# Kernel optimization log

Hardware: AMD Instinct MI355X
Metric: run time of the kernel (lower is better)

## Reference

```python
import jax, jax.numpy as jnp
import numpy as np
import math

EPS = 1e-6

def _rmsnorm(x, w):
    var = jnp.mean(x * x, axis=-1, keepdims=True)
    return x * jax.lax.rsqrt(var + EPS) * w

def _rotary(x, cos, sin):
    d = x.shape[-1] // 2
    x1, x2 = x[..., :d], x[..., d:]
    return jnp.concatenate([x1 * cos - x2 * sin, x2 * cos + x1 * sin], axis=-1)

def _conv1x1(x, w):
    # x: (B, C, 1, S), w: (O, C) -> (B, O, 1, S)
    return jnp.einsum('bcls,oc->bols', x, w)

def setup_inputs() -> dict:
    key = jax.random.key(0)
    ks = jax.random.split(key, 12)
    B, H, KVH, D, S, T, HID = 8, 16, 2, 128, 16, 8192, 2048
    return {
        'x': jax.random.normal(ks[0], (B, HID, 1, S), jnp.float32),
        'cos': jax.random.uniform(ks[1], (1, 1, S, D // 2), jnp.float32),
        'sin': jax.random.uniform(ks[2], (1, 1, S, D // 2), jnp.float32),
        'kv_cache_k': jax.random.normal(ks[3], (B, KVH, T, D), jnp.float32),
        'kv_cache_v': jax.random.normal(ks[4], (B, KVH, T, D), jnp.float32),
        'position': 4096,
        'mask': jnp.zeros((1, 1, S, T), jnp.float32),
        'wq': jax.random.normal(ks[5], (H * D, HID), jnp.float32) * 0.02,
        'wk': jax.random.normal(ks[6], (KVH * D, HID), jnp.float32) * 0.02,
        'wv': jax.random.normal(ks[7], (KVH * D, HID), jnp.float32) * 0.02,
        'wo': jax.random.normal(ks[8], (HID, H * D), jnp.float32) * 0.02,
        'q_norm_w': jnp.ones((D,), jnp.float32),
        'k_norm_w': jnp.ones((D,), jnp.float32),
    }

def reference(x, cos, sin, kv_cache_k, kv_cache_v, position, mask,
              wq, wk, wv, wo, q_norm_w, k_norm_w):
    B, S = x.shape[0], x.shape[3]
    D = q_norm_w.shape[0]
    H = wq.shape[0] // D
    KVH = wk.shape[0] // D
    G = H // KVH  # GQA group size

    # projections (1x1 conv == channel matmul), then (B, h, S, D)
    q = _conv1x1(x, wq)[:, :, 0, :].reshape(B, H, D, S).transpose(0, 1, 3, 2)
    k = _conv1x1(x, wk)[:, :, 0, :].reshape(B, KVH, D, S).transpose(0, 1, 3, 2)
    v = _conv1x1(x, wv)[:, :, 0, :].reshape(B, KVH, D, S).transpose(0, 1, 3, 2)

    q = _rotary(_rmsnorm(q, q_norm_w), cos, sin)
    k = _rotary(_rmsnorm(k, k_norm_w), cos, sin)

    # scatter new k/v into cache at `position`
    new_k = jax.lax.dynamic_update_slice(kv_cache_k, k, (0, 0, position, 0))
    new_v = jax.lax.dynamic_update_slice(kv_cache_v, v, (0, 0, position, 0))

    # GQA: fold q heads into (kv_head, group) so K/V need no repeat_interleave
    scale = 1.0 / math.sqrt(D)
    qg = q.reshape(B, KVH, G, S, D)
    attn = jnp.einsum('bkgsd,bktd->bkgst', qg, new_k) * scale
    attn = attn + mask[:, :, None, :, :]  # (1,1,S,T) -> broadcast over groups
    probs = jax.nn.softmax(attn, axis=-1)
    out = jnp.einsum('bkgst,bktd->bkgsd', probs, new_v).reshape(B, H, S, D)

    # back to (B, H*D, 1, S) and output projection
    out = out.transpose(0, 1, 3, 2).reshape(B, H * D, 1, S)
    out = _conv1x1(out, wo)
    return out, new_k, new_v
```

## Files before the change

### kernel.cpp

```cpp
#include <hip/hip_runtime.h>
#include <cstdint>
#include <cstddef>


typedef __attribute__((ext_vector_type(8))) short bf16x8;
typedef __attribute__((ext_vector_type(4))) float f32x4;
typedef unsigned short u16;
typedef unsigned int u32;

#define MFMA16(a, b, c) __builtin_amdgcn_mfma_f32_16x16x32_bf16(a, b, c, 0, 0, 0)

static __device__ __forceinline__ u16 f2bf(float f) {
  u32 u = __float_as_uint(f);
  u += 0x7FFFu + ((u >> 16) & 1u);
  return (u16)(u >> 16);
}
static __device__ __forceinline__ float bf2f(u16 u) {
  return __uint_as_float(((u32)u) << 16);
}
static __device__ __forceinline__ u32 pk2(float a, float b) {
  return (u32)f2bf(a) | ((u32)f2bf(b) << 16);
}

__global__ __launch_bounds__(256) void transpose_x(const float* __restrict__ x,
                                                   u16* __restrict__ Xt) {
  int id = blockIdx.x * 256 + threadIdx.x;
  int b = id >> 13, c = (id >> 2) & 2047, s4 = id & 3;
  float4 v = *(const float4*)(x + ((size_t)(b * 2048 + c)) * 16 + s4 * 4);
  size_t base = (size_t)(b * 16 + s4 * 4) * 2048 + c;
  Xt[base]        = f2bf(v.x);
  Xt[base + 2048] = f2bf(v.y);
  Xt[base + 4096] = f2bf(v.z);
  Xt[base + 6144] = f2bf(v.w);
}

template <int MODE>
__global__ __launch_bounds__(512) void gemm16(const float* __restrict__ w0,
                                              const float* __restrict__ w1,
                                              const float* __restrict__ w2,
                                              const u16* __restrict__ Bt,
                                              float* __restrict__ outp) {
  __shared__ __align__(16) u16 sW[2][16 * 256];
  __shared__ __align__(16) float sRed[2048];
  const int t512 = threadIdx.x;
  const int half = t512 >> 8;
  const int tid = t512 & 255;
  const int lane = tid & 63, w = tid >> 6;
  const int q = lane >> 4, n = lane & 15;
  const int m0 = blockIdx.x * 16;
  const float* wbase;
  if (MODE == 0) {
    if (m0 < 2048)      wbase = w0 + (size_t)m0 * 2048;
    else if (m0 < 2304) wbase = w1 + (size_t)(m0 - 2048) * 2048;
    else                wbase = w2 + (size_t)(m0 - 2304) * 2048;
  } else {
    wbase = w0 + (size_t)m0 * 2048;
  }
  const int kbase = half * 1024;
  f32x4 acc0 = {0.f, 0.f, 0.f, 0.f}, acc1 = acc0;

  for (int c0 = kbase; c0 < kbase + 1024; c0 += 256) {
    {
      int m = tid >> 4, s16 = tid & 15;
      const float* src = wbase + (size_t)m * 2048 + c0 + s16 * 16;
      float4 a = *(const float4*)(src);
      float4 b = *(const float4*)(src + 4);
      float4 c = *(const float4*)(src + 8);
      float4 d = *(const float4*)(src + 12);
      uint4 u0 = {pk2(a.x, a.y), pk2(a.z, a.w), pk2(b.x, b.y), pk2(b.z, b.w)};
      uint4 u1 = {pk2(c.x, c.y), pk2(c.z, c.w), pk2(d.x, d.y), pk2(d.z, d.w)};
      int G0 = 2 * s16;
      *(uint4*)&sW[half][m * 256 + ((G0 + m) & 31) * 8]     = u0;
      *(uint4*)&sW[half][m * 256 + ((G0 + 1 + m) & 31) * 8] = u1;
    }
    __syncthreads();
    bf16x8 bfr[2][8];
#pragma unroll
    for (int e = 0; e < 2; ++e) {
      int j = 32 * w + 16 * e + n;
      const u16* bp = Bt + (size_t)j * 2048 + c0 + q * 8;
#pragma unroll
      for (int ks = 0; ks < 8; ++ks) bfr[e][ks] = *(const bf16x8*)(bp + ks * 32);
    }
#pragma unroll
    for (int ks = 0; ks < 8; ++ks) {
      bf16x8 af = *(const bf16x8*)&sW[half][n * 256 + (((4 * ks + q) + n) & 31) * 8];
      acc0 = MFMA16(af, bfr[0][ks], acc0);
      acc1 = MFMA16(af, bfr[1][ks], acc1);
    }
    __syncthreads();
  }
  if (half == 1) {
    *(f32x4*)&sRed[tid * 8]     = acc0;
    *(f32x4*)&sRed[tid * 8 + 4] = acc1;
  }
  __syncthreads();
  if (half == 0) {
    acc0 += *(const f32x4*)&sRed[tid * 8];
    acc1 += *(const f32x4*)&sRed[tid * 8 + 4];
#pragma unroll
    for (int e = 0; e < 2; ++e) {
      f32x4 a = e ? acc1 : acc0;
      int j = 32 * w + 16 * e + n;
      if (MODE == 0) {
        *(f32x4*)&outp[(size_t)j * 2560 + m0 + 4 * q] = a;
      } else {
#pragma unroll
        for (int reg = 0; reg < 4; ++reg) {
          int m = m0 + 4 * q + reg;
          outp[(size_t)(j >> 4) * 32768 + m * 16 + (j & 15)] = a[reg];
        }
      }
    }
  }
}

__global__ __launch_bounds__(256) void norm_rot(
    const float* __restrict__ qkv, const float* __restrict__ cosb,
    const float* __restrict__ sinb, const float* __restrict__ qw,
    const float* __restrict__ kw,
    u16* __restrict__ Qa, float* __restrict__ knew, float* __restrict__ vnew) {
  const int wid = blockIdx.x * 4 + (threadIdx.x >> 6);
  const int lane = threadIdx.x & 63;
  const float SCALE = 0.08838834764831845f;
  if (wid < 2048) {
    int b = wid >> 8, h = (wid >> 4) & 15, s = wid & 15;
    int j = b * 16 + s;
    const float* row = qkv + (size_t)j * 2560 + h * 128;
    float v1 = row[lane];
    float v2 = row[lane + 64];
    float ss = v1 * v1 + v2 * v2;
#pragma unroll
    for (int o = 32; o > 0; o >>= 1) ss += __shfl_xor(ss, o, 64);
    float rr = rsqrtf(ss * (1.0f / 128.0f) + 1e-6f);
    float n1 = v1 * rr * qw[lane];
    float n2 = v2 * rr * qw[lane + 64];
    float c = cosb[s * 64 + lane], sn = sinb[s * 64 + lane];
    u16* dst = Qa + (size_t)((b * 16 + h) * 16 + s) * 128;
    dst[lane]      = f2bf((n1 * c - n2 * sn) * SCALE);
    dst[lane + 64] = f2bf((n2 * c + n1 * sn) * SCALE);
  } else if (wid < 2304) {
    int idx = wid - 2048;
    int b = idx >> 5, kvh = (idx >> 4) & 1, s = idx & 15;
    int j = b * 16 + s;
    const float* row = qkv + (size_t)j * 2560 + 2048 + kvh * 128;
    float v1 = row[lane];
    float v2 = row[lane + 64];
    float ss = v1 * v1 + v2 * v2;
#pragma unroll
    for (int o = 32; o > 0; o >>= 1) ss += __shfl_xor(ss, o, 64);
    float rr = rsqrtf(ss * (1.0f / 128.0f) + 1e-6f);
    float n1 = v1 * rr * kw[lane];
    float n2 = v2 * rr * kw[lane + 64];
    float c = cosb[s * 64 + lane], sn = sinb[s * 64 + lane];
    float* dst = knew + (size_t)((b * 2 + kvh) * 16 + s) * 128;
    dst[lane]      = n1 * c - n2 * sn;
    dst[lane + 64] = n2 * c + n1 * sn;
  } else {
    int idx = wid - 2304;
    int b = idx >> 5, kvh = (idx >> 4) & 1, s = idx & 15;
    int j = b * 16 + s;
    const float* row = qkv + (size_t)j * 2560 + 2304 + kvh * 128;
    float* dst = vnew + (size_t)((b * 2 + kvh) * 16 + s) * 128;
    dst[lane]      = row[lane];
    dst[lane + 64] = row[lane + 64];
  }
}

__global__ __launch_bounds__(256, 2) void attn(
    const u16* __restrict__ Qa, const float* __restrict__ kcache,
    const float* __restrict__ vcache, const float* __restrict__ knew,
    const float* __restrict__ vnew, const int* __restrict__ posp,
    const float* __restrict__ mask, float* __restrict__ outk,
    float* __restrict__ outv, u16* __restrict__ Opart,
    float* __restrict__ Mpart, float* __restrict__ Lpart) {
  __shared__ __align__(16) u16 lds[32768];

  const int tid = threadIdx.x, lane = tid & 63, w = tid >> 6;
  const int q = lane >> 4, n = lane & 15;
  const int bid = blockIdx.x;
  const int bk = bid >> 5, chunk = bid & 31;
  const int b = bk >> 1, kvh = bk & 1;
  const int pos = *posp;

  const int stl = tid >> 4;
  const int g = tid & 15;

#define SRC_PTR(isV_, tg_)                                                   \
  ((isV_) ? (((tg_) >= pos && (tg_) < pos + 16)                              \
                 ? (vnew + (size_t)(bk * 16 + ((tg_) - pos)) * 128)          \
                 : (vcache + ((size_t)bk * 8192 + (tg_)) * 128))             \
          : (((tg_) >= pos && (tg_) < pos + 16)                              \
                 ? (knew + (size_t)(bk * 16 + ((tg_) - pos)) * 128)          \
                 : (kcache + ((size_t)bk * 8192 + (tg_)) * 128)))

  float4 pf[8][2];
#define ISSUE_STAGE(tile_)                                                   \
  {                                                                          \
    const int t0_ = chunk * 256 + (tile_) * 64;                              \
    _Pragma("unroll") for (int u = 0; u < 8; ++u) {                          \
      int isV_ = u >> 2;                                                     \
      int tl_ = (stl + 16 * u) & 63;                                         \
      int tg_ = t0_ + tl_;                                                   \
      const float* s_ = SRC_PTR(isV_, tg_) + g * 8;                          \
      pf[u][0] = *(const float4*)(s_);                                       \
      pf[u][1] = *(const float4*)(s_ + 4);                                   \
    }                                                                        \
  }

  float4 mv4[4];
#define LOAD_MASK(tile_)                                                     \
  {                                                                          \
    const int t0_ = chunk * 256 + (tile_) * 64;                              \
    _Pragma("unroll") for (int mt = 0; mt < 4; ++mt)                         \
        mv4[mt] =                                                            \
        *(const float4*)(mask + (size_t)n * 8192 + t0_ + 16 * mt + 4 * q);   \
  }

  ISSUE_STAGE(0);

  bf16x8 qf[2][4];
#pragma unroll
  for (int e = 0; e < 2; ++e) {
    int r = 32 * w + 16 * e + n;
    int h = kvh * 8 + (r >> 4), s = r & 15;
    const u16* qrow = Qa + (size_t)((b * 16 + h) * 16 + s) * 128;
#pragma unroll
    for (int ks = 0; ks < 4; ++ks)
      qf[e][ks] = *(const bf16x8*)(qrow + (4 * ks + q) * 8);
  }

  LOAD_MASK(0);

  bf16x8 idE = {0, 0, 0, 0, 0, 0, 0, 0}, idO = idE;
  {
    const short one = (short)0x3F80;
    int tq = n >> 3, te = n & 7;
#pragma unroll
    for (int e = 0; e < 8; ++e) {
      if (q == tq && e == te) idE[e] = one;
      if (q == tq + 2 && e == te) idO[e] = one;
    }
  }

  float m_old[2] = {-INFINITY, -INFINITY}, l_old[2] = {0.f, 0.f};
  f32x4 oacc[2][8];
#pragma unroll
  for (int e = 0; e < 2; ++e)
#pragma unroll
    for (int nt = 0; nt < 8; ++nt) oacc[e][nt] = (f32x4){0.f, 0.f, 0.f, 0.f};

  for (int tile = 0; tile < 4; ++tile) {
    const int t0 = chunk * 256 + tile * 64;
#pragma unroll
    for (int u = 0; u < 8; ++u) {
      int isV = u >> 2;
      int tl = (stl + 16 * u) & 63;
      int tg = t0 + tl;
      float* dst = (isV ? outv : outk) + ((size_t)bk * 8192 + tg) * 128 + g * 8;
      float4 a = pf[u][0], b2 = pf[u][1];
      *(float4*)dst = a;
      *(float4*)(dst + 4) = b2;
      uint4 uu = {pk2(a.x, a.y), pk2(a.z, a.w), pk2(b2.x, b2.y), pk2(b2.z, b2.w)};
      *(uint4*)&lds[isV * 8192 + tl * 128 + ((g + tl) & 15) * 8] = uu;
    }
    __syncthreads();

    if (tile < 3) { ISSUE_STAGE(tile + 1); }

    f32x4 sacc[4][2];
#pragma unroll
    for (int mt = 0; mt < 4; ++mt) {
      sacc[mt][0] = (f32x4){0.f, 0.f, 0.f, 0.f};
      sacc[mt][1] = sacc[mt][0];
    }
#pragma unroll
    for (int ks = 0; ks < 4; ++ks) {
#pragma unroll
      for (int mt = 0; mt < 4; ++mt) {
        int trow = 16 * mt + n;
        bf16x8 kf = *(const bf16x8*)&lds[trow * 128 + (((4 * ks + q) + trow) & 15) * 8];
        sacc[mt][0] = MFMA16(kf, qf[0][ks], sacc[mt][0]);
        sacc[mt][1] = MFMA16(kf, qf[1][ks], sacc[mt][1]);
      }
    }

#pragma unroll
    for (int mtv = 0; mtv < 4; ++mtv) {
      int trow = 16 * mtv + n;
      bf16x8 vfr = *(const bf16x8*)&lds[8192 + trow * 128 + (((4 * w + q) + trow) & 15) * 8];
      f32x4 z = {0.f, 0.f, 0.f, 0.f};
      f32x4 d0 = MFMA16(vfr, idE, z);
      f32x4 d1 = MFMA16(vfr, idO, z);
      int G = 2 * mtv + (q >> 1), off = 4 * (q & 1);
      int dp0 = 32 * w + n, dp1 = dp0 + 16;
      uint2 u0 = {pk2(d0[0], d0[1]), pk2(d0[2], d0[3])};
      uint2 u1 = {pk2(d1[0], d1[1]), pk2(d1[2], d1[3])};
      *(uint2*)&lds[24576 + dp0 * 64 + ((G + dp0) & 7) * 8 + off] = u0;
      *(uint2*)&lds[24576 + dp1 * 64 + ((G + dp1) & 7) * 8 + off] = u1;
    }

    float al[2];
#pragma unroll
    for (int e = 0; e < 2; ++e) {
      float sv[4][4];
      float mx = -INFINITY;
#pragma unroll
      for (int mt = 0; mt < 4; ++mt)
#pragma unroll
        for (int rg = 0; rg < 4; ++rg) {
          float v = sacc[mt][e][rg] + mv4[mt][rg];
          sv[mt][rg] = v;
          mx = fmaxf(mx, v);
        }
      mx = fmaxf(mx, __shfl_xor(mx, 16));
      mx = fmaxf(mx, __shfl_xor(mx, 32));
      float mn = fmaxf(m_old[e], mx);
      al[e] = __expf(m_old[e] - mn);
      float ts = 0.f;
      int r = 32 * w + 16 * e + n;
#pragma unroll
      for (int mt = 0; mt < 4; ++mt) {
        float p0 = __expf(sv[mt][0] - mn), p1 = __expf(sv[mt][1] - mn);
        float p2 = __expf(sv[mt][2] - mn), p3 = __expf(sv[mt][3] - mn);
        ts += (p0 + p1) + (p2 + p3);
        uint2 up = {pk2(p0, p1), pk2(p2, p3)};
        int G = 2 * mt + (q >> 1), off = 4 * (q & 1);
        *(uint2*)&lds[16384 + r * 64 + ((G + r) & 7) * 8 + off] = up;
      }
      ts += __shfl_xor(ts, 16);
      ts += __shfl_xor(ts, 32);
      l_old[e] = l_old[e] * al[e] + ts;
      m_old[e] = mn;
    }
    if (tile < 3) { LOAD_MASK(tile + 1); }
    __syncthreads();

#pragma unroll
    for (int e = 0; e < 2; ++e) {
      float an[4];
#pragma unroll
      for (int rg = 0; rg < 4; ++rg) an[rg] = __shfl(al[e], 4 * q + rg);
#pragma unroll
      for (int nt = 0; nt < 8; ++nt)
#pragma unroll
        for (int rg = 0; rg < 4; ++rg) oacc[e][nt][rg] *= an[rg];
    }
    bf16x8 Pf[2][2];
#pragma unroll
    for (int e = 0; e < 2; ++e) {
      int r = 32 * w + 16 * e + n;
#pragma unroll
      for (int ks = 0; ks < 2; ++ks)
        Pf[e][ks] = *(const bf16x8*)&lds[16384 + r * 64 + (((4 * ks + q) + r) & 7) * 8];
    }
#pragma unroll
    for (int nt = 0; nt < 8; ++nt) {
      int d = 16 * nt + n;
#pragma unroll
      for (int ks = 0; ks < 2; ++ks) {
        bf16x8 vf = *(const bf16x8*)&lds[24576 + d * 64 + (((4 * ks + q) + d) & 7) * 8];
        oacc[0][nt] = MFMA16(Pf[0][ks], vf, oacc[0][nt]);
        oacc[1][nt] = MFMA16(Pf[1][ks], vf, oacc[1][nt]);
      }
    }
  }

#pragma unroll
  for (int e = 0; e < 2; ++e)
#pragma unroll
    for (int nt = 0; nt < 8; ++nt) {
      int d = 16 * nt + n;
      int r0 = 32 * w + 16 * e + 4 * q;
      int G = r0 >> 3, off = 4 * (q & 1);
      uint2 u = {pk2(oacc[e][nt][0], oacc[e][nt][1]),
                 pk2(oacc[e][nt][2], oacc[e][nt][3])};
      *(uint2*)&lds[d * 128 + ((G + d) & 15) * 8 + off] = u;
    }
  if (q == 0) {
#pragma unroll
    for (int e = 0; e < 2; ++e) {
      int r = 32 * w + 16 * e + n;
      Mpart[(size_t)bid * 128 + r] = m_old[e];
      Lpart[(size_t)bid * 128 + r] = l_old[e];
    }
  }
  __syncthreads();
  for (int i = tid; i < 2048; i += 256) {
    int d2 = i >> 4, g2 = i & 15;
    uint4 v = *(const uint4*)&lds[d2 * 128 + ((g2 + d2) & 15) * 8];
    *(uint4*)(Opart + (size_t)bid * 16384 + d2 * 128 + g2 * 8) = v;
  }
#undef SRC_PTR
#undef ISSUE_STAGE
#undef LOAD_MASK
}

__global__ __launch_bounds__(256) void combine(const u16* __restrict__ Opart,
                                               const float* __restrict__ Mp,
                                               const float* __restrict__ Lp,
                                               u16* __restrict__ A2t) {
  __shared__ float wgt[32 * 128];
  const int tid = threadIdx.x;
  const int bk = blockIdx.x, dgrp = blockIdx.y;
  if (tid < 128) {
    int r = tid;
    float mc[32], M = -INFINITY;
#pragma unroll
    for (int c = 0; c < 32; ++c) {
      mc[c] = Mp[(size_t)(bk * 32 + c) * 128 + r];
      M = fmaxf(M, mc[c]);
    }
    float L = 0.f, wv[32];
#pragma unroll
    for (int c = 0; c < 32; ++c) {
      wv[c] = __expf(mc[c] - M);
      L += wv[c] * Lp[(size_t)(bk * 32 + c) * 128 + r];
    }
    float inv = 1.0f / L;
#pragma unroll
    for (int c = 0; c < 32; ++c) wgt[c * 128 + r] = wv[c] * inv;
  }
  __syncthreads();
  int r = tid & 127, dd = tid >> 7;
  int b = bk >> 1, kvh = bk & 1;
  int h = kvh * 8 + (r >> 4), s = r & 15;
  size_t arow = (size_t)(b * 16 + s) * 2048 + h * 128;
  for (int di = 0; di < 8; ++di) {
    int d = dgrp * 16 + dd + 2 * di;
    float o = 0.f;
#pragma unroll
    for (int c = 0; c < 32; ++c)
      o += wgt[c * 128 + r] *
           bf2f(Opart[((size_t)(bk * 32 + c) * 128 + d) * 128 + r]);
    A2t[arow + d] = f2bf(o);
  }
}

extern "C" void kernel_launch(void* const* d_in, const int* in_sizes, int n_in,
                              void* d_out, int out_size, void* d_ws, size_t ws_size,
                              hipStream_t stream) {
  const float* x    = (const float*)d_in[0];
  const float* cosb = (const float*)d_in[1];
  const float* sinb = (const float*)d_in[2];
  const float* kc   = (const float*)d_in[3];
  const float* vc   = (const float*)d_in[4];
  const int*   posp = (const int*)d_in[5];
  const float* mask = (const float*)d_in[6];
  const float* wq   = (const float*)d_in[7];
  const float* wk   = (const float*)d_in[8];
  const float* wv   = (const float*)d_in[9];
  const float* wo   = (const float*)d_in[10];
  const float* qw   = (const float*)d_in[11];
  const float* kw   = (const float*)d_in[12];

  float* out  = (float*)d_out;
  float* outk = out + 262144;
  float* outv = outk + 16777216;

  float* ws      = (float*)d_ws;
  float* ws_qkv  = ws;
  float* ws_knew = ws + 327680;
  float* ws_vnew = ws + 360448;
  u16*   ws_Qa   = (u16*)(ws + 393216);
  u16*   ws_Xt   = (u16*)(ws + 524288);
  u16*   ws_A2t  = (u16*)(ws + 655360);
  float* ws_M    = ws + 786432;
  float* ws_L    = ws + 851968;
  u16*   ws_O    = (u16*)(ws + 917504);

  transpose_x<<<256, 256, 0, stream>>>(x, ws_Xt);
  gemm16<0><<<160, 512, 0, stream>>>(wq, wk, wv, ws_Xt, ws_qkv);
  norm_rot<<<640, 256, 0, stream>>>(ws_qkv, cosb, sinb, qw, kw,
                                    ws_Qa, ws_knew, ws_vnew);
  attn<<<512, 256, 0, stream>>>(ws_Qa, kc, vc, ws_knew, ws_vnew, posp, mask,
                                outk, outv, ws_O, ws_M, ws_L);
  combine<<<dim3(16, 8), 256, 0, stream>>>(ws_O, ws_M, ws_L, ws_A2t);
  gemm16<1><<<128, 512, 0, stream>>>(wo, wo, wo, ws_A2t, out);
}
```

Before: 365.9 us.

## Raise attention occupancy by dropping register prefetch and P LDS staging

The attention kernel drops its register-held software prefetch of the next K/V tile and mask. K/V and the mask are now loaded directly inside each tile iteration. The P fragment is assembled through cross-lane shuffles instead of an LDS round trip, which shrinks LDS to 48KB and, together with fewer registers, allows 3 blocks per CU instead of 2. MFMA sections are wrapped in s_setprio. The combine kernel gets twice as many blocks, each accumulating 4 output columns at once. The trade is losing explicit load/compute overlap within a block in exchange for more resident waves hiding latency.

```diff
diff --git a/kernel.cpp b/kernel.cpp
--- a/kernel.cpp
+++ b/kernel.cpp
@@ -167,14 +167,14 @@
   }
 }
 
-__global__ __launch_bounds__(256, 2) void attn(
+__global__ __launch_bounds__(256, 3) void attn(
     const u16* __restrict__ Qa, const float* __restrict__ kcache,
     const float* __restrict__ vcache, const float* __restrict__ knew,
     const float* __restrict__ vnew, const int* __restrict__ posp,
     const float* __restrict__ mask, float* __restrict__ outk,
     float* __restrict__ outv, u16* __restrict__ Opart,
     float* __restrict__ Mpart, float* __restrict__ Lpart) {
-  __shared__ __align__(16) u16 lds[32768];
+  __shared__ __align__(16) u16 lds[24576];
 
   const int tid = threadIdx.x, lane = tid & 63, w = tid >> 6;
   const int q = lane >> 4, n = lane & 15;
@@ -182,42 +182,8 @@
   const int bk = bid >> 5, chunk = bid & 31;
   const int b = bk >> 1, kvh = bk & 1;
   const int pos = *posp;
-
   const int stl = tid >> 4;
   const int g = tid & 15;
-
-#define SRC_PTR(isV_, tg_)                                                   \
-  ((isV_) ? (((tg_) >= pos && (tg_) < pos + 16)                              \
-                 ? (vnew + (size_t)(bk * 16 + ((tg_) - pos)) * 128)          \
-                 : (vcache + ((size_t)bk * 8192 + (tg_)) * 128))             \
-          : (((tg_) >= pos && (tg_) < pos + 16)                              \
-                 ? (knew + (size_t)(bk * 16 + ((tg_) - pos)) * 128)          \
-                 : (kcache + ((size_t)bk * 8192 + (tg_)) * 128)))
-
-  float4 pf[8][2];
-#define ISSUE_STAGE(tile_)                                                   \
-  {                                                                          \
-    const int t0_ = chunk * 256 + (tile_) * 64;                              \
-    _Pragma("unroll") for (int u = 0; u < 8; ++u) {                          \
-      int isV_ = u >> 2;                                                     \
-      int tl_ = (stl + 16 * u) & 63;                                         \
-      int tg_ = t0_ + tl_;                                                   \
-      const float* s_ = SRC_PTR(isV_, tg_) + g * 8;                          \
-      pf[u][0] = *(const float4*)(s_);                                       \
-      pf[u][1] = *(const float4*)(s_ + 4);                                   \
-    }                                                                        \
-  }
-
-  float4 mv4[4];
-#define LOAD_MASK(tile_)                                                     \
-  {                                                                          \
-    const int t0_ = chunk * 256 + (tile_) * 64;                              \
-    _Pragma("unroll") for (int mt = 0; mt < 4; ++mt)                         \
-        mv4[mt] =                                                            \
-        *(const float4*)(mask + (size_t)n * 8192 + t0_ + 16 * mt + 4 * q);   \
-  }
-
-  ISSUE_STAGE(0);
 
   bf16x8 qf[2][4];
 #pragma unroll
@@ -230,8 +196,6 @@
       qf[e][ks] = *(const bf16x8*)(qrow + (4 * ks + q) * 8);
   }
 
-  LOAD_MASK(0);
-
   bf16x8 idE = {0, 0, 0, 0, 0, 0, 0, 0}, idO = idE;
   {
     const short one = (short)0x3F80;
@@ -257,8 +221,18 @@
       int isV = u >> 2;
       int tl = (stl + 16 * u) & 63;
       int tg = t0 + tl;
+      const float* src;
+      if (!isV)
+        src = (tg >= pos && tg < pos + 16)
+                  ? (knew + (size_t)(bk * 16 + (tg - pos)) * 128)
+                  : (kcache + ((size_t)bk * 8192 + tg) * 128);
+      else
+        src = (tg >= pos && tg < pos + 16)
+                  ? (vnew + (size_t)(bk * 16 + (tg - pos)) * 128)
+                  : (vcache + ((size_t)bk * 8192 + tg) * 128);
       float* dst = (isV ? outv : outk) + ((size_t)bk * 8192 + tg) * 128 + g * 8;
-      float4 a = pf[u][0], b2 = pf[u][1];
+      float4 a = *(const float4*)(src + g * 8);
+      float4 b2 = *(const float4*)(src + g * 8 + 4);
       *(float4*)dst = a;
       *(float4*)(dst + 4) = b2;
       uint4 uu = {pk2(a.x, a.y), pk2(a.z, a.w), pk2(b2.x, b2.y), pk2(b2.z, b2.w)};
@@ -266,7 +240,10 @@
     }
     __syncthreads();
 
-    if (tile < 3) { ISSUE_STAGE(tile + 1); }
+    float4 mv4[4];
+#pragma unroll
+    for (int mt = 0; mt < 4; ++mt)
+      mv4[mt] = *(const float4*)(mask + (size_t)n * 8192 + t0 + 16 * mt + 4 * q);
 
     f32x4 sacc[4][2];
 #pragma unroll
@@ -274,6 +251,7 @@
       sacc[mt][0] = (f32x4){0.f, 0.f, 0.f, 0.f};
       sacc[mt][1] = sacc[mt][0];
     }
+    __builtin_amdgcn_s_setprio(1);
 #pragma unroll
     for (int ks = 0; ks < 4; ++ks) {
 #pragma unroll
@@ -284,6 +262,7 @@
         sacc[mt][1] = MFMA16(kf, qf[1][ks], sacc[mt][1]);
       }
     }
+    __builtin_amdgcn_s_setprio(0);
 
 #pragma unroll
     for (int mtv = 0; mtv < 4; ++mtv) {
@@ -296,11 +275,12 @@
       int dp0 = 32 * w + n, dp1 = dp0 + 16;
       uint2 u0 = {pk2(d0[0], d0[1]), pk2(d0[2], d0[3])};
       uint2 u1 = {pk2(d1[0], d1[1]), pk2(d1[2], d1[3])};
-      *(uint2*)&lds[24576 + dp0 * 64 + ((G + dp0) & 7) * 8 + off] = u0;
-      *(uint2*)&lds[24576 + dp1 * 64 + ((G + dp1) & 7) * 8 + off] = u1;
+      *(uint2*)&lds[16384 + dp0 * 64 + ((G + dp0) & 7) * 8 + off] = u0;
+      *(uint2*)&lds[16384 + dp1 * 64 + ((G + dp1) & 7) * 8 + off] = u1;
     }
 
     float al[2];
+    bf16x8 Pf[2][2];
 #pragma unroll
     for (int e = 0; e < 2; ++e) {
       float sv[4][4];
@@ -318,52 +298,58 @@
       float mn = fmaxf(m_old[e], mx);
       al[e] = __expf(m_old[e] - mn);
       float ts = 0.f;
-      int r = 32 * w + 16 * e + n;
+      u32 U[4][2];
 #pragma unroll
       for (int mt = 0; mt < 4; ++mt) {
         float p0 = __expf(sv[mt][0] - mn), p1 = __expf(sv[mt][1] - mn);
         float p2 = __expf(sv[mt][2] - mn), p3 = __expf(sv[mt][3] - mn);
         ts += (p0 + p1) + (p2 + p3);
-        uint2 up = {pk2(p0, p1), pk2(p2, p3)};
-        int G = 2 * mt + (q >> 1), off = 4 * (q & 1);
-        *(uint2*)&lds[16384 + r * 64 + ((G + r) & 7) * 8 + off] = up;
+        U[mt][0] = pk2(p0, p1);
+        U[mt][1] = pk2(p2, p3);
       }
       ts += __shfl_xor(ts, 16);
       ts += __shfl_xor(ts, 32);
       l_old[e] = l_old[e] * al[e] + ts;
       m_old[e] = mn;
-    }
-    if (tile < 3) { LOAD_MASK(tile + 1); }
+      const int srcbase = n + ((q & 1) << 5);
+#pragma unroll
+      for (int ks = 0; ks < 2; ++ks) {
+        u32 pw[4];
+#pragma unroll
+        for (int i = 0; i < 4; ++i) {
+          int src = srcbase + ((i >> 1) << 4);
+          u32 lo = (u32)__shfl((int)U[2 * ks][i & 1], src, 64);
+          u32 hi = (u32)__shfl((int)U[2 * ks + 1][i & 1], src, 64);
+          pw[i] = (q >> 1) ? hi : lo;
+        }
+        uint4 pv = {pw[0], pw[1], pw[2], pw[3]};
+        Pf[e][ks] = __builtin_bit_cast(bf16x8, pv);
+      }
+    }
     __syncthreads();
 
 #pragma unroll
     for (int e = 0; e < 2; ++e) {
       float an[4];
 #pragma unroll
-      for (int rg = 0; rg < 4; ++rg) an[rg] = __shfl(al[e], 4 * q + rg);
+      for (int rg = 0; rg < 4; ++rg) an[rg] = __shfl(al[e], 4 * q + rg, 64);
 #pragma unroll
       for (int nt = 0; nt < 8; ++nt)
 #pragma unroll
         for (int rg = 0; rg < 4; ++rg) oacc[e][nt][rg] *= an[rg];
     }
-    bf16x8 Pf[2][2];
-#pragma unroll
-    for (int e = 0; e < 2; ++e) {
-      int r = 32 * w + 16 * e + n;
-#pragma unroll
-      for (int ks = 0; ks < 2; ++ks)
-        Pf[e][ks] = *(const bf16x8*)&lds[16384 + r * 64 + (((4 * ks + q) + r) & 7) * 8];
-    }
+    __builtin_amdgcn_s_setprio(1);
 #pragma unroll
     for (int nt = 0; nt < 8; ++nt) {
       int d = 16 * nt + n;
 #pragma unroll
       for (int ks = 0; ks < 2; ++ks) {
-        bf16x8 vf = *(const bf16x8*)&lds[24576 + d * 64 + (((4 * ks + q) + d) & 7) * 8];
+        bf16x8 vf = *(const bf16x8*)&lds[16384 + d * 64 + (((4 * ks + q) + d) & 7) * 8];
         oacc[0][nt] = MFMA16(Pf[0][ks], vf, oacc[0][nt]);
         oacc[1][nt] = MFMA16(Pf[1][ks], vf, oacc[1][nt]);
       }
     }
+    __builtin_amdgcn_s_setprio(0);
   }
 
 #pragma unroll
@@ -391,9 +377,6 @@
     uint4 v = *(const uint4*)&lds[d2 * 128 + ((g2 + d2) & 15) * 8];
     *(uint4*)(Opart + (size_t)bid * 16384 + d2 * 128 + g2 * 8) = v;
   }
-#undef SRC_PTR
-#undef ISSUE_STAGE
-#undef LOAD_MASK
 }
 
 __global__ __launch_bounds__(256) void combine(const u16* __restrict__ Opart,
@@ -426,14 +409,21 @@
   int b = bk >> 1, kvh = bk & 1;
   int h = kvh * 8 + (r >> 4), s = r & 15;
   size_t arow = (size_t)(b * 16 + s) * 2048 + h * 128;
-  for (int di = 0; di < 8; ++di) {
-    int d = dgrp * 16 + dd + 2 * di;
-    float o = 0.f;
-#pragma unroll
-    for (int c = 0; c < 32; ++c)
-      o += wgt[c * 128 + r] *
-           bf2f(Opart[((size_t)(bk * 32 + c) * 128 + d) * 128 + r]);
-    A2t[arow + d] = f2bf(o);
+  float o[4] = {0.f, 0.f, 0.f, 0.f};
+#pragma unroll
+  for (int c = 0; c < 32; ++c) {
+    float wv = wgt[c * 128 + r];
+    size_t base = ((size_t)(bk * 32 + c) * 128) * 128 + r;
+#pragma unroll
+    for (int di = 0; di < 4; ++di) {
+      int d = dgrp * 8 + dd + 2 * di;
+      o[di] += wv * bf2f(Opart[base + (size_t)d * 128]);
+    }
+  }
+#pragma unroll
+  for (int di = 0; di < 4; ++di) {
+    int d = dgrp * 8 + dd + 2 * di;
+    A2t[arow + d] = f2bf(o[di]);
   }
 }
 
@@ -475,6 +465,6 @@
                                     ws_Qa, ws_knew, ws_vnew);
   attn<<<512, 256, 0, stream>>>(ws_Qa, kc, vc, ws_knew, ws_vnew, posp, mask,
                                 outk, outv, ws_O, ws_M, ws_L);
-  combine<<<dim3(16, 8), 256, 0, stream>>>(ws_O, ws_M, ws_L, ws_A2t);
+  combine<<<dim3(16, 16), 256, 0, stream>>>(ws_O, ws_M, ws_L, ws_A2t);
   gemm16<1><<<128, 512, 0, stream>>>(wo, wo, wo, ws_A2t, out);
 }
```

New measurement: 386.0 us. +5.5%, slower.
